# Performance work log

Hardware: AMD Instinct MI355X
Metric: run time of the kernel (lower is better)

The kernel has to match this reference:

```python
import jax, jax.numpy as jnp
import numpy as np

NH = 25            # nHidden
NS = 20            # nStep (MPC horizon)
DT = 1.0 / 60.0    # del_t
EPS = 1e-4
PQ = 5.0           # terminal cost weight
QV = 200.0         # velocity cost weight
QA = 1.0           # control cost weight
BATCH = 131072
D = NH + 2         # augmented state dim


def setup_inputs() -> dict:
    key = jax.random.key(0)
    k1, k2, k3, k4, k5 = jax.random.split(key, 5)
    x = jax.random.normal(k1, (BATCH, NH), jnp.float32)
    gripper_p = jax.random.normal(k2, (BATCH,), jnp.float32)
    gripper_v = jax.random.normal(k3, (BATCH,), jnp.float32)
    # learned parameters of the module
    Af = jax.random.uniform(k4, (NH, 1), jnp.float32)               # feature->position coupling column
    Lq = jnp.tril(jax.random.uniform(k5, (NH, NH), jnp.float32))    # Cholesky-style factor of Q0
    return {"x": x, "gripper_p": gripper_p, "gripper_v": gripper_v, "Af": Af, "Lq": Lq}


def _build_system(Af, Lq):
    """Assemble the (batch-shared) MPC matrices: Q_final, p_final, S_, T_."""
    eyeD = jnp.eye(D, dtype=Af.dtype)
    # A0 = [[I, 0, Af], [0 .. 0, [1 dt; 0 1]]]
    top = jnp.concatenate([jnp.eye(NH, dtype=Af.dtype), jnp.zeros((NH, 1), Af.dtype), Af], axis=1)
    ap = jnp.concatenate([jnp.zeros((2, NH), Af.dtype),
                          jnp.array([[1.0, DT], [0.0, 1.0]], Af.dtype)], axis=1)
    A0 = jnp.concatenate([top, ap], axis=0)                                   # [D, D]
    B0 = jnp.concatenate([jnp.zeros((NH, 1), Af.dtype),
                          jnp.array([[0.5 * DT * DT], [DT]], Af.dtype)], axis=0)  # [D, 1]
    # stage cost Q0 (padded with [0 0; 0 Qv] block)
    Q0 = Lq @ Lq.T + EPS * jnp.eye(NH, dtype=Af.dtype)
    Q0f = (jnp.zeros((D, D), Af.dtype)
           .at[:NH, :NH].set(Q0)
           .at[NH:, NH:].set(jnp.array([[0.0, 0.0], [0.0, QV]], Af.dtype)))
    # powers A0^0..A0^NS (small fixed loop, NS=20)
    pows = [eyeD]
    for _ in range(NS):
        pows.append(pows[-1] @ A0)
    P = jnp.stack(pows)                    # [NS+1, D, D]
    T_ = P[1:].reshape(NS * D, D)          # stacked A0^1..A0^NS
    # S_ block (r,c) = A0^(r-c) @ B0 for c<=r (block lower-triangular), else 0
    SB = P @ B0                            # [NS+1, D, 1]
    r = jnp.arange(NS)
    diff = r[:, None] - r[None, :]         # [NS, NS]
    Sblk = jnp.where((diff >= 0)[:, :, None, None], SB[jnp.clip(diff, 0)], 0.0)  # [NS, NS, D, 1]
    S_ = Sblk.transpose(0, 2, 1, 3).reshape(NS * D, NS)
    # block-diagonal Q (last block scaled by Pq)
    Qblocks = jnp.concatenate([jnp.tile(Q0f[None], (NS - 1, 1, 1)), PQ * Q0f[None]], axis=0)
    Qd = jnp.zeros((NS, D, NS, D), Af.dtype).at[r, :, r, :].set(Qblocks).reshape(NS * D, NS * D)
    QS = Qd @ S_                                                       # [NS*D, NS]
    Q_final = 2.0 * (QA * jnp.eye(NS, dtype=Af.dtype) + S_.T @ QS) + EPS * jnp.eye(NS, dtype=Af.dtype)
    p_final = 2.0 * (T_.T @ QS)                                        # [D, NS]
    return Q_final, p_final, S_, T_


def reference(x, gripper_p, gripper_v, Af, Lq):
    nB = x.shape[0]
    Q_final, p_final, S_, T_ = _build_system(Af, Lq)
    x0 = jnp.concatenate([x, gripper_p[:, None], gripper_v[:, None]], axis=1)  # [B, D]
    p = x0 @ p_final                                                           # [B, NS]
    # QP with G=0, h=0 (trivially satisfied) and no equality constraints ->
    # unconstrained minimizer: u = -Q_final^{-1} p
    u = -jnp.linalg.solve(Q_final, p.T).T                                      # [B, NS]
    x_predict = u @ S_.T + x0 @ T_.T                                           # [B, NS*D]
    # output selector picks the gripper position entry (index NH) of each block
    return x_predict.reshape(nB, NS, D)[:, :, NH]                              # [B, NS]
```

## Files before the change

kernel.cpp:

```cpp
#include <hip/hip_runtime.h>

#define NHID 25
#define NSTEP 20
#define DT_ (1.0f/60.0f)
#define EPS_ 1e-4f
#define PQ_ 5.0f
#define QV_ 200.0f
#define QA_ 1.0f
#define NAUG (NSTEP + 2)
#define NEL  (NSTEP * NAUG)

__global__ __launch_bounds__(256) void mpc_fused(
    const float* __restrict__ x, const float* __restrict__ gp,
    const float* __restrict__ gv, const float* __restrict__ Af,
    const float* __restrict__ Lq, float* __restrict__ out)
{
    __shared__ float xs[256 * NHID];
    __shared__ float Lqs[NHID * NHID];
    __shared__ float Afs[NHID];
    __shared__ float wv_[NHID];
    __shared__ float us[NHID];
    __shared__ float alpha_s;
    __shared__ float aug[NSTEP][NAUG + 2];
    __shared__ float bs[NSTEP];
    __shared__ float gs[NSTEP];

    const int t = threadIdx.x;
    const size_t b0 = (size_t)blockIdx.x * 256;
    const float dt = DT_;

    if (t < NHID) Afs[t] = Af[t];
    for (int i = t; i < NHID * NHID; i += 256) Lqs[i] = Lq[i];
    {
        const float4* xsrc = (const float4*)(x + b0 * NHID);
        float4* xdst = (float4*)xs;
        #pragma unroll
        for (int i = 0; i < 7; ++i) {
            int idx = t + 256 * i;
            if (idx < 1600) xdst[idx] = xsrc[idx];
        }
    }
    const float p = gp[b0 + t];
    const float v = gv[b0 + t];
    __syncthreads();

    if (t < NHID) {
        float acc = 0.0f;
        for (int i = t; i < NHID; ++i)
            acc = fmaf(Lqs[i * NHID + t], Afs[i], acc);
        wv_[t] = acc;
    }
    __syncthreads();
    if (t < NHID) {
        float acc = EPS_ * Afs[t];
        for (int j = 0; j <= t; ++j)
            acc = fmaf(Lqs[t * NHID + j], wv_[j], acc);
        us[t] = acc;
    }
    __syncthreads();
    if (t == 0) {
        float a = 0.0f;
        for (int i = 0; i < NHID; ++i) a = fmaf(Afs[i], us[i], a);
        alpha_s = a;
    }
    __syncthreads();
    const float alpha = alpha_s;

    for (int idx = t; idx < NEL; idx += 256) {
        int r = idx / NAUG, c = idx % NAUG;
        float val;
        if (c < NSTEP) {
            int m0 = (r > c) ? r : c;
            float s = 0.0f;
            for (int rr = m0; rr < NSTEP; ++rr) {
                float wr = (rr == NSTEP - 1) ? PQ_ : 1.0f;
                s = fmaf(wr, fmaf((float)(rr - r) * (float)(rr - c), alpha, QV_), s);
            }
            val = 2.0f * dt * dt * s + ((r == c) ? (2.0f * QA_ + EPS_) : 0.0f);
        } else if (c == NSTEP) {
            float s = 0.0f;
            for (int rr = r; rr < NSTEP; ++rr)
                s += ((rr == NSTEP - 1) ? PQ_ : 1.0f) * (float)(rr - r);
            val = s;
        } else {
            float s = 0.0f;
            for (int rr = r; rr < NSTEP; ++rr) {
                float wr = (rr == NSTEP - 1) ? PQ_ : 1.0f;
                s = fmaf(wr, fmaf((float)(rr + 1) * (float)(rr - r), alpha, QV_), s);
            }
            val = s;
        }
        aug[r][c] = val;
    }
    __syncthreads();

    const int r0 = t / NAUG,        c0 = t % NAUG;
    const int r1 = (t + 256) / NAUG, c1 = (t + 256) % NAUG;
    for (int piv = 0; piv < NSTEP; ++piv) {
        float app  = aug[piv][piv];
        float pinv = 1.0f / app;
        float n0 = 0.0f, n1 = 0.0f;
        if (t < NEL) {
            float arc = aug[r0][c0], apc = aug[piv][c0], arp = aug[r0][piv];
            n0 = (r0 == piv) ? arc * pinv : fmaf(-arp * pinv, apc, arc);
        }
        if (t < NEL - 256) {
            float arc = aug[r1][c1], apc = aug[piv][c1], arp = aug[r1][piv];
            n1 = (r1 == piv) ? arc * pinv : fmaf(-arp * pinv, apc, arc);
        }
        __syncthreads();
        if (t < NEL)       aug[r0][c0] = n0;
        if (t < NEL - 256) aug[r1][c1] = n1;
        __syncthreads();
    }

    if (t < NSTEP) {
        const float hdt2 = 0.5f * dt * dt;
        float bacc = 0.0f, gacc = 0.0f;
        for (int c = 0; c <= t; ++c) {
            float ssel = fmaf((float)(t - c), dt * dt, hdt2);
            bacc = fmaf(aug[c][NSTEP],     ssel, bacc);
            gacc = fmaf(aug[c][NSTEP + 1], ssel, gacc);
        }
        bs[t] = -2.0f * dt * bacc;
        gs[t] = fmaf((float)(t + 1), dt, -2.0f * dt * gacc);
    }
    __syncthreads();

    const float* xr = xs + t * NHID;
    float tb = 0.0f;
    #pragma unroll
    for (int i = 0; i < NHID; ++i)
        tb = fmaf(xr[i], us[i], tb);

    float4* o4 = (float4*)(out + (b0 + t) * NSTEP);
    #pragma unroll
    for (int q = 0; q < 5; ++q) {
        float4 r;
        r.x = fmaf(tb, bs[4*q+0], fmaf(v, gs[4*q+0], p));
        r.y = fmaf(tb, bs[4*q+1], fmaf(v, gs[4*q+1], p));
        r.z = fmaf(tb, bs[4*q+2], fmaf(v, gs[4*q+2], p));
        r.w = fmaf(tb, bs[4*q+3], fmaf(v, gs[4*q+3], p));
        o4[q] = r;
    }
}

extern "C" void kernel_launch(void* const* d_in, const int* in_sizes, int n_in,
                              void* d_out, int out_size, void* d_ws, size_t ws_size,
                              hipStream_t stream) {
    const float* x  = (const float*)d_in[0];
    const float* gp = (const float*)d_in[1];
    const float* gv = (const float*)d_in[2];
    const float* Af = (const float*)d_in[3];
    const float* Lq = (const float*)d_in[4];
    float* out = (float*)d_out;

    const int B = in_sizes[1];
    hipLaunchKernelGGL(mpc_fused, dim3(B / 256), dim3(256), 0, stream,
                       x, gp, gv, Af, Lq, out);
}
```

Baseline: 86.38 us.

## Split batch-shared MPC system solve into single-block setup kernel

Moves the batch-independent work (Q0/Af reductions, 20x22 Gauss-Jordan solve, selector coefficients) out of every block into a one-block setup kernel that writes the constants to workspace. The streaming kernel then only loads x, gp, gv and the constants and does the per-row dot product and output. This removes redundant per-block serial elimination with its many barriers. The cost is an extra launch with a serialized one-block dependency.

```diff
diff --git a/kernel.cpp b/kernel.cpp
--- a/kernel.cpp
+++ b/kernel.cpp
@@ -10,38 +10,23 @@
 #define NAUG (NSTEP + 2)
 #define NEL  (NSTEP * NAUG)
 
-__global__ __launch_bounds__(256) void mpc_fused(
-    const float* __restrict__ x, const float* __restrict__ gp,
-    const float* __restrict__ gv, const float* __restrict__ Af,
-    const float* __restrict__ Lq, float* __restrict__ out)
+
+__global__ __launch_bounds__(256) void mpc_setup(
+    const float* __restrict__ Af, const float* __restrict__ Lq,
+    float* __restrict__ cst)
 {
-    __shared__ float xs[256 * NHID];
     __shared__ float Lqs[NHID * NHID];
     __shared__ float Afs[NHID];
     __shared__ float wv_[NHID];
     __shared__ float us[NHID];
     __shared__ float alpha_s;
     __shared__ float aug[NSTEP][NAUG + 2];
-    __shared__ float bs[NSTEP];
-    __shared__ float gs[NSTEP];
 
     const int t = threadIdx.x;
-    const size_t b0 = (size_t)blockIdx.x * 256;
     const float dt = DT_;
 
     if (t < NHID) Afs[t] = Af[t];
     for (int i = t; i < NHID * NHID; i += 256) Lqs[i] = Lq[i];
-    {
-        const float4* xsrc = (const float4*)(x + b0 * NHID);
-        float4* xdst = (float4*)xs;
-        #pragma unroll
-        for (int i = 0; i < 7; ++i) {
-            int idx = t + 256 * i;
-            if (idx < 1600) xdst[idx] = xsrc[idx];
-        }
-    }
-    const float p = gp[b0 + t];
-    const float v = gv[b0 + t];
     __syncthreads();
 
     if (t < NHID) {
@@ -94,7 +79,7 @@
     }
     __syncthreads();
 
-    const int r0 = t / NAUG,        c0 = t % NAUG;
+    const int r0 = t / NAUG,         c0 = t % NAUG;
     const int r1 = (t + 256) / NAUG, c1 = (t + 256) % NAUG;
     for (int piv = 0; piv < NSTEP; ++piv) {
         float app  = aug[piv][piv];
@@ -122,9 +107,43 @@
             bacc = fmaf(aug[c][NSTEP],     ssel, bacc);
             gacc = fmaf(aug[c][NSTEP + 1], ssel, gacc);
         }
-        bs[t] = -2.0f * dt * bacc;
-        gs[t] = fmaf((float)(t + 1), dt, -2.0f * dt * gacc);
+        cst[NHID + t]         = -2.0f * dt * bacc;
+        cst[NHID + NSTEP + t] = fmaf((float)(t + 1), dt, -2.0f * dt * gacc);
     }
+    if (t < NHID) cst[t] = us[t];
+}
+
+__global__ __launch_bounds__(256) void mpc_stream(
+    const float* __restrict__ x, const float* __restrict__ gp,
+    const float* __restrict__ gv, const float* __restrict__ cst,
+    float* __restrict__ out)
+{
+    __shared__ float xs[256 * NHID];
+    __shared__ float us[NHID];
+    __shared__ float bs[NSTEP];
+    __shared__ float gs[NSTEP];
+
+    const int t = threadIdx.x;
+    const size_t b0 = (size_t)blockIdx.x * 256;
+
+    if (t < NHID + 2 * NSTEP) {
+        float c = cst[t];
+        if (t < NHID)              us[t] = c;
+        else if (t < NHID + NSTEP) bs[t - NHID] = c;
+        else                       gs[t - NHID - NSTEP] = c;
+    }
+
+    {
+        const float4* xsrc = (const float4*)(x + b0 * NHID);
+        float4* xdst = (float4*)xs;
+        #pragma unroll
+        for (int i = 0; i < 7; ++i) {
+            int idx = t + 256 * i;
+            if (idx < 1600) xdst[idx] = xsrc[idx];
+        }
+    }
+    const float p = gp[b0 + t];
+    const float v = gv[b0 + t];
     __syncthreads();
 
     const float* xr = xs + t * NHID;
@@ -154,8 +173,11 @@
     const float* Af = (const float*)d_in[3];
     const float* Lq = (const float*)d_in[4];
     float* out = (float*)d_out;
+    float* cst = (float*)d_ws;
 
     const int B = in_sizes[1];
-    hipLaunchKernelGGL(mpc_fused, dim3(B / 256), dim3(256), 0, stream,
-                       x, gp, gv, Af, Lq, out);
+
+    hipLaunchKernelGGL(mpc_setup, dim3(1), dim3(256), 0, stream, Af, Lq, cst);
+    hipLaunchKernelGGL(mpc_stream, dim3(B / 256), dim3(256), 0, stream,
+                       x, gp, gv, cst, out);
 }
```

Measured after the change: 89.15 us. 1.03x slower.
